# Kernel optimization log

Measured on AMD Instinct MI355X. Metric: run time of the kernel, lower is better.

Reference implementation:

```python
import jax, jax.numpy as jnp
import numpy as np

N = 20000   # nodes
IN = 128    # in_feats
H = 2       # n_heads
D = 32      # per-head dim (hid_feats = H*D = 64)
K = 3       # diffusion hops in AGDNConv
R = 5       # relations into dst type 'drug'
E = 320000  # edges per relation
NEG_SLOPE = 0.2


def setup_inputs() -> dict:
    key = jax.random.key(0)
    ks = jax.random.split(key, 11)
    s = 1.0 / np.sqrt(IN)
    return dict(
        h=jax.random.normal(ks[0], (N, IN), jnp.float32),
        src_idx=jax.random.randint(ks[1], (R, E), 0, N, dtype=jnp.int32),
        dst_idx=jax.random.randint(ks[2], (R, E), 0, N, dtype=jnp.int32),
        fc_w=jax.random.normal(ks[3], (R, IN, H * D), jnp.float32) * s,
        res_w=jax.random.normal(ks[4], (R, IN, H * D), jnp.float32) * s,
        attn_l=jax.random.normal(ks[5], (R, H, D), jnp.float32) * 0.1,
        attn_r=jax.random.normal(ks[6], (R, H, D), jnp.float32) * 0.1,
        hop_attn_l=jax.random.normal(ks[7], (R, H, D), jnp.float32) * 0.1,
        hop_attn_r=jax.random.normal(ks[8], (R, H, D), jnp.float32) * 0.1,
        w_rel=jax.random.normal(ks[9], (R, R), jnp.float32) * (1.0 / np.sqrt(R)),
        b_rel=jax.random.normal(ks[10], (R,), jnp.float32) * 0.1,
    )


def _agdn_conv(h, src, dst, fc_w, res_w, al, ar, hal, har):
    """One AGDNConv (GAT attention + K-hop diffusion + HA hop attention + residual)."""
    x = (h @ fc_w).reshape(N, H, D)                       # [N,H,D] projected feats
    el = jnp.sum(x * al, -1)                              # [N,H]
    er = jnp.sum(x * ar, -1)                              # [N,H]
    e = jax.nn.leaky_relu(el[src] + er[dst], NEG_SLOPE)   # [E,H] edge logits
    # segment softmax over incoming edges per dst node
    emax = jax.ops.segment_max(e, dst, num_segments=N)
    emax = jnp.where(jnp.isfinite(emax), emax, 0.0)
    ee = jnp.exp(e - emax[dst])
    denom = jax.ops.segment_sum(ee, dst, num_segments=N)
    alpha = ee / jnp.maximum(denom[dst], 1e-9)            # [E,H]

    def hop(hk, _):
        msg = alpha[:, :, None] * hk[src]                 # [E,H,D] gather+weight
        hk1 = jax.ops.segment_sum(msg, dst, num_segments=N)
        return hk1, hk1

    _, hks = jax.lax.scan(hop, x, None, length=K)         # [K,N,H,D]
    hops = jnp.concatenate([x[None], hks], axis=0)        # [K+1,N,H,D]
    # hop_norm: L2 normalize each hop's features
    hops = hops / jnp.maximum(jnp.linalg.norm(hops, axis=-1, keepdims=True), 1e-9)
    # HA hop attention
    hl = jnp.sum(hops * hal, -1)                          # [K+1,N,H]
    hr = jnp.sum(hops[0] * har, -1)                       # [N,H]
    hop_w = jax.nn.softmax(jax.nn.leaky_relu(hl + hr[None], NEG_SLOPE), axis=0)
    out = jnp.einsum('knh,knhd->nhd', hop_w, hops)        # [N,H,D]
    return out + (h @ res_w).reshape(N, H, D)             # residual


def reference(h, src_idx, dst_idx, fc_w, res_w, attn_l, attn_r, hop_attn_l, hop_attn_r, w_rel, b_rel):
    # per-relation AGDN convolutions (HeteroGraphConv dispatch)
    outs = jax.vmap(_agdn_conv, in_axes=(None, 0, 0, 0, 0, 0, 0, 0, 0))(
        h, src_idx, dst_idx, fc_w, res_w, attn_l, attn_r, hop_attn_l, hop_attn_r)  # [R,N,H,D]
    # my_agg_func2: learned relation weights = model_drug(ones(R))
    weights = w_rel @ jnp.ones((R,), jnp.float32) + b_rel  # [R]
    combined = jnp.einsum('r,rnhd->nhd', weights, outs)    # weighted relation sum
    return jnp.mean(combined, axis=1)                      # combine='mean' over heads -> [N,D]
```

## Files before the change

kernel.cpp:

```cpp
#include <hip/hip_runtime.h>
#include <hip/hip_bf16.h>

#define NN 20000
#define IN 128
#define HH 2
#define DD 32
#define HD 64
#define KK 3
#define RR 5
#define EE 320000
#define NEG 0.2f

#define PADK 136
#define NB 313
#define NBLK 64
#define CHUNK 5000
#define CAP 2048
#define NBCAP (NB * CAP)
#define RPS 20004
#define HTOT (NN * IN / 4)

typedef short v8s __attribute__((ext_vector_type(8)));
typedef float v4f __attribute__((ext_vector_type(4)));
typedef _Float16 hf8 __attribute__((ext_vector_type(8)));

__device__ __forceinline__ ushort f2b(float f) {
    unsigned u = __float_as_uint(f);
    unsigned r = (u + 0x7fff + ((u >> 16) & 1)) >> 16;
    return (ushort)r;
}
__device__ __forceinline__ ushort f2h(float f) {
    _Float16 h = (_Float16)f;
    return __builtin_bit_cast(ushort, h);
}
__device__ __forceinline__ float h2f(ushort u) {
    _Float16 h = __builtin_bit_cast(_Float16, u);
    return (float)h;
}
__device__ __forceinline__ float2 up2(unsigned u) {
    return make_float2(h2f((ushort)(u & 0xFFFF)), h2f((ushort)(u >> 16)));
}

__global__ __launch_bounds__(256) void cvt_kernel(
    const float* __restrict__ h, const float* __restrict__ fcw,
    const float* __restrict__ resw, ushort* __restrict__ wb,
    ushort* __restrict__ hb, int* __restrict__ bcnt)
{
    int j = blockIdx.x * 256 + threadIdx.x;
    if (j < RR * NB) bcnt[j] = 0;
    if (j < RR * 128 * IN) {
        int k = j & 127;
        int c = (j >> 7) & 127;
        int r = j >> 14;
        float v = (c < HD) ? fcw[(r * IN + k) * HD + c] : resw[(r * IN + k) * HD + (c - HD)];
        wb[j] = f2b(v);
    }
    int t = j - RR * 128 * IN;
    if (t >= 0 && t < HTOT) {
        float4 v = ((const float4*)h)[t];
        ((ushort4*)hb)[t] = make_ushort4(f2b(v.x), f2b(v.y), f2b(v.z), f2b(v.w));
    }
}

__global__ __launch_bounds__(256) void proj_mfma(
    const ushort* __restrict__ hb, const ushort* __restrict__ wb,
    const float* __restrict__ attn_l, const float* __restrict__ attn_r,
    ushort* __restrict__ t0, ushort* __restrict__ resh,
    float* __restrict__ el, float* __restrict__ er)
{
    __shared__ ushort As[64 * PADK];
    __shared__ ushort Bs[128 * PADK];
    int bx = blockIdx.x;
    int r = bx / 313;
    int tile = bx - r * 313;
    int n0 = tile * 64;
    int tid = threadIdx.x;

    #pragma unroll
    for (int i = 0; i < 4; i++) {
        int c = tid + 256 * i;
        int row = c >> 4;
        int off = (c & 15) * 8;
        int gn = n0 + row;
        uint4 v = make_uint4(0u, 0u, 0u, 0u);
        if (gn < NN) v = *(const uint4*)&hb[(size_t)gn * IN + off];
        *(uint4*)&As[row * PADK + off] = v;
    }
    const ushort* wr = wb + (size_t)r * 128 * IN;
    #pragma unroll
    for (int i = 0; i < 8; i++) {
        int c = tid + 256 * i;
        int row = c >> 4;
        int off = (c & 15) * 8;
        *(uint4*)&Bs[row * PADK + off] = *(const uint4*)&wr[row * IN + off];
    }
    __syncthreads();

    int w = tid >> 6, lane = tid & 63;
    int lm = lane & 15, lq = lane >> 4;

    v4f acc[4][2];
    #pragma unroll
    for (int mt = 0; mt < 4; mt++)
        #pragma unroll
        for (int nt = 0; nt < 2; nt++) acc[mt][nt] = (v4f){0.f, 0.f, 0.f, 0.f};

    const ushort* Ab = &As[lm * PADK + lq * 8];
    const ushort* Bb = &Bs[(w * 32 + lm) * PADK + lq * 8];

    #pragma unroll
    for (int ks = 0; ks < 4; ks++) {
        v8s a[4], b[2];
        #pragma unroll
        for (int mt = 0; mt < 4; mt++) a[mt] = *(const v8s*)(Ab + mt * 16 * PADK + ks * 32);
        #pragma unroll
        for (int nt = 0; nt < 2; nt++) b[nt] = *(const v8s*)(Bb + nt * 16 * PADK + ks * 32);
        #pragma unroll
        for (int mt = 0; mt < 4; mt++)
            #pragma unroll
            for (int nt = 0; nt < 2; nt++)
                acc[mt][nt] = __builtin_amdgcn_mfma_f32_16x16x32_bf16(a[mt], b[nt], acc[mt][nt], 0, 0, 0);
    }

    int colbase = w * 32 + lm;
    #pragma unroll
    for (int mt = 0; mt < 4; mt++) {
        #pragma unroll
        for (int nt = 0; nt < 2; nt++) {
            int col = colbase + nt * 16;
            #pragma unroll
            for (int p = 0; p < 4; p++) {
                int node = n0 + mt * 16 + lq * 4 + p;
                if (node < NN) {
                    float v = acc[mt][nt][p];
                    if (col < HD) {
                        t0[((size_t)r * NN + node) * HD + col] = f2h(v);
                    } else {
                        resh[((size_t)r * NN + node) * HD + (col - HD)] = f2h(v);
                    }
                }
            }
        }
    }

    if (w < 2) {
        float al0 = attn_l[(r * HH + w) * DD + lm];
        float al1 = attn_l[(r * HH + w) * DD + lm + 16];
        float ar0 = attn_r[(r * HH + w) * DD + lm];
        float ar1 = attn_r[(r * HH + w) * DD + lm + 16];
        #pragma unroll
        for (int mt = 0; mt < 4; mt++) {
            #pragma unroll
            for (int p = 0; p < 4; p++) {
                float pl = acc[mt][0][p] * al0 + acc[mt][1][p] * al1;
                float pr = acc[mt][0][p] * ar0 + acc[mt][1][p] * ar1;
                #pragma unroll
                for (int off = 1; off < 16; off <<= 1) {
                    pl += __shfl_xor(pl, off, 64);
                    pr += __shfl_xor(pr, off, 64);
                }
                if (lm == 0) {
                    int node = n0 + mt * 16 + lq * 4 + p;
                    if (node < NN) {
                        el[((size_t)r * NN + node) * HH + w] = pl;
                        er[((size_t)r * NN + node) * HH + w] = pr;
                    }
                }
            }
        }
    }
}

__global__ __launch_bounds__(256) void part_kernel(
    const int* __restrict__ src, const int* __restrict__ dst,
    int* __restrict__ bcnt, unsigned* __restrict__ bucketRec)
{
    __shared__ int hh[NB];
    int r = blockIdx.x >> 6;
    int blk = blockIdx.x & 63;
    int tid = threadIdx.x;
    for (int i = tid; i < NB; i += 256) hh[i] = 0;
    __syncthreads();
    const int* S = src + (size_t)r * EE + blk * CHUNK;
    const int* D = dst + (size_t)r * EE + blk * CHUNK;
    for (int i = tid; i < CHUNK; i += 256)
        atomicAdd(&hh[D[i] >> 6], 1);
    __syncthreads();
    for (int i = tid; i < NB; i += 256) {
        int c = hh[i];
        hh[i] = c ? atomicAdd(&bcnt[r * NB + i], c) : 0;
    }
    __syncthreads();
    unsigned* BR = bucketRec + (size_t)r * NBCAP;
    for (int i = tid; i < CHUNK; i += 256) {
        int s = S[i], d = D[i];
        int b = d >> 6;
        int pos = atomicAdd(&hh[b], 1);
        if (pos < CAP)
            BR[((size_t)b << 11) + pos] = (unsigned)s | ((unsigned)(d & 63) << 15);
    }
}

__global__ __launch_bounds__(256) void bsort_alpha_kernel(
    const unsigned* __restrict__ bucketRec, const int* __restrict__ bcnt,
    const float* __restrict__ el, const float* __restrict__ er,
    uint2* __restrict__ csrE, int* __restrict__ rowp)
{
    __shared__ int cnt64s[4][64];
    __shared__ int segS[65];
    __shared__ int cur[64];
    __shared__ float2 erL[64];
    __shared__ float2 mx2[64];
    __shared__ float2 inv2[64];
    __shared__ unsigned sSD[CAP];
    __shared__ unsigned sL[CAP];

    int bk = blockIdx.x;
    int r = bk / NB;
    int bkt = bk - r * NB;
    int tid = threadIdx.x;
    int wv = tid >> 6;
    int cnt = bcnt[bk];
    if (cnt > CAP) cnt = CAP;

    if (tid < 64) {
        cnt64s[0][tid] = 0; cnt64s[1][tid] = 0;
        cnt64s[2][tid] = 0; cnt64s[3][tid] = 0;
        int gn = bkt * 64 + tid;
        erL[tid] = (gn < NN) ? ((const float2*)er)[(size_t)r * NN + gn]
                             : make_float2(0.f, 0.f);
    }
    __syncthreads();
    const unsigned* BR = bucketRec + (size_t)bk * CAP;
    for (int i = tid; i < cnt; i += 256)
        atomicAdd(&cnt64s[wv][(BR[i] >> 15) & 63], 1);
    __syncthreads();
    if (tid < 64) {
        int v = cnt64s[0][tid] + cnt64s[1][tid] + cnt64s[2][tid] + cnt64s[3][tid];
        int x = v;
        #pragma unroll
        for (int off = 1; off < 64; off <<= 1) {
            int tt = __shfl_up(x, off, 64);
            if (tid >= off) x += tt;
        }
        segS[tid] = x - v;
        cur[tid] = x - v;
        if (tid == 63) segS[64] = x;
    }
    __syncthreads();
    const float2* el2 = (const float2*)el + (size_t)r * NN;
    for (int i = tid; i < cnt; i += 256) {
        unsigned rec = BR[i];
        int s = rec & 0x7FFF;
        int d = (rec >> 15) & 63;
        float2 a = el2[s];
        float2 b = erL[d];
        float l0 = a.x + b.x; l0 = l0 > 0.f ? l0 : NEG * l0;
        float l1 = a.y + b.y; l1 = l1 > 0.f ? l1 : NEG * l1;
        int pos = atomicAdd(&cur[d], 1);
        sSD[pos] = rec;
        sL[pos] = (unsigned)f2h(l0) | ((unsigned)f2h(l1) << 16);
    }
    __syncthreads();
    {
        int d = tid >> 2, sub = tid & 3;
        int b0 = segS[d], e0 = segS[d + 1];
        float m0 = -1e30f, m1 = -1e30f;
        for (int i = b0 + sub; i < e0; i += 4) {
            float2 l = up2(sL[i]);
            m0 = fmaxf(m0, l.x); m1 = fmaxf(m1, l.y);
        }
        m0 = fmaxf(m0, __shfl_xor(m0, 1, 64));
        m0 = fmaxf(m0, __shfl_xor(m0, 2, 64));
        m1 = fmaxf(m1, __shfl_xor(m1, 1, 64));
        m1 = fmaxf(m1, __shfl_xor(m1, 2, 64));
        float s0 = 0.f, s1 = 0.f;
        for (int i = b0 + sub; i < e0; i += 4) {
            float2 l = up2(sL[i]);
            s0 += __expf(l.x - m0); s1 += __expf(l.y - m1);
        }
        s0 += __shfl_xor(s0, 1, 64); s0 += __shfl_xor(s0, 2, 64);
        s1 += __shfl_xor(s1, 1, 64); s1 += __shfl_xor(s1, 2, 64);
        if (sub == 0) {
            mx2[d] = make_float2(m0, m1);
            inv2[d] = make_float2(1.f / fmaxf(s0, 1e-9f), 1.f / fmaxf(s1, 1e-9f));
            int gn = bkt * 64 + d;
            if (gn < NN) {
                int len = e0 - b0;
                rowp[r * RPS + gn] = (int)(((unsigned)(bkt * CAP + b0)) | ((unsigned)len << 20));
            }
        }
    }
    __syncthreads();
    uint2* E = csrE + (size_t)bk * CAP;
    for (int i = tid; i < cnt; i += 256) {
        unsigned rec = sSD[i];
        int d = (rec >> 15) & 63;
        float2 l = up2(sL[i]);
        float w0 = __expf(l.x - mx2[d].x) * inv2[d].x;
        float w1 = __expf(l.y - mx2[d].y) * inv2[d].y;
        E[i] = make_uint2(rec, (unsigned)f2h(w0) | ((unsigned)f2h(w1) << 16));
    }
}

__global__ __launch_bounds__(256) void hop_kernel(
    const ushort* __restrict__ tin, ushort* __restrict__ tout,
    const uint2* __restrict__ csrE, const int* __restrict__ rowp)
{
    int nbk = gridDim.x;
    int q = nbk >> 3, rmd = nbk & 7;
    int xcd = blockIdx.x & 7, pos = blockIdx.x >> 3;
    int bid = (xcd < rmd ? xcd * (q + 1) : rmd * (q + 1) + (xcd - rmd) * q) + pos;

    int w = (bid * 256 + (int)threadIdx.x) >> 6;
    if (w >= RR * (NN / 8)) return;
    int lane = threadIdx.x & 63;
    int g = lane >> 3;
    int f = (lane & 7) * 8;
    int sh = ((lane >> 2) & 1) * 16;
    int r = w / (NN / 8);
    int n0 = (w - r * (NN / 8)) * 8;

    unsigned pv = (unsigned)rowp[r * RPS + n0 + g];
    int bg = (int)(pv & 0xFFFFF);
    int len = (int)(pv >> 20);
    int eg = bg + len;
    int cl = (len + 1) >> 1;
    int b2 = bg + cl;

    int lastA = bg + cl - 1;
    lastA = lastA > bg ? lastA : bg;
    int lastB = eg - 1;
    lastB = lastB > b2 ? lastB : b2;

    const ushort* T = tin + (size_t)r * NN * HD;
    const uint2* E = csrE + (size_t)r * NBCAP;

    int iA1 = bg + 1 < lastA ? bg + 1 : lastA;
    int iB1 = b2 + 1 < lastB ? b2 + 1 : lastB;
    uint2 raC = E[lastA < bg ? lastA : bg], rbC = E[b2 < lastB ? b2 : lastB];
    uint2 raN = E[iA1], rbN = E[iB1];
    int na0 = (int)(raC.x & 0x7FFF); na0 = na0 < NN ? na0 : 0;
    int nb0 = (int)(rbC.x & 0x7FFF); nb0 = nb0 < NN ? nb0 : 0;
    hf8 fa = *(const hf8*)&T[(size_t)na0 * HD + f];
    hf8 fb = *(const hf8*)&T[(size_t)nb0 * HD + f];

    float accA[8] = {0.f, 0.f, 0.f, 0.f, 0.f, 0.f, 0.f, 0.f};
    float accB[8] = {0.f, 0.f, 0.f, 0.f, 0.f, 0.f, 0.f, 0.f};
    #pragma unroll 2
    for (int j = 0; j < cl; j++) {
        int ja = bg + j + 2; ja = ja < lastA ? ja : lastA;
        int jb = b2 + j + 2; jb = jb < lastB ? jb : lastB;
        uint2 ra2 = E[ja];
        uint2 rb2 = E[jb];
        int na1 = (int)(raN.x & 0x7FFF); na1 = na1 < NN ? na1 : 0;
        int nb1 = (int)(rbN.x & 0x7FFF); nb1 = nb1 < NN ? nb1 : 0;
        hf8 fa1 = *(const hf8*)&T[(size_t)na1 * HD + f];
        hf8 fb1 = *(const hf8*)&T[(size_t)nb1 * HD + f];
        float wa = h2f((ushort)(raC.y >> sh));
        float wb = (b2 + j < eg) ? h2f((ushort)(rbC.y >> sh)) : 0.f;
        #pragma unroll
        for (int k2 = 0; k2 < 8; k2++) {
            accA[k2] += wa * (float)fa[k2];
            accB[k2] += wb * (float)fb[k2];
        }
        raC = raN; raN = ra2;
        rbC = rbN; rbN = rb2;
        fa = fa1; fb = fb1;
    }
    ushort o[8];
    #pragma unroll
    for (int k = 0; k < 8; k++) o[k] = f2h(accA[k] + accB[k]);
    *(uint4*)&tout[((size_t)r * NN + n0 + g) * HD + f] = *(uint4*)o;
}

__global__ __launch_bounds__(256) void final_kernel(
    const ushort* __restrict__ t0, const ushort* __restrict__ t1,
    const ushort* __restrict__ t2, const ushort* __restrict__ t3,
    const ushort* __restrict__ resh,
    const float* __restrict__ hal, const float* __restrict__ har,
    const float* __restrict__ w_rel, const float* __restrict__ b_rel,
    float* __restrict__ out)
{
    int idx = blockIdx.x * 256 + threadIdx.x;
    if (idx >= NN * HH * 4) return;
    int fq = idx & 3;
    int h_ = (idx >> 2) & 1;
    int n = idx >> 3;
    const ushort* tb[4] = {t0, t1, t2, t3};
    float o[8];
    #pragma unroll
    for (int d = 0; d < 8; d++) o[d] = 0.f;

    for (int r = 0; r < RR; r++) {
        float wr = b_rel[r];
        #pragma unroll
        for (int j = 0; j < RR; j++) wr += w_rel[r * RR + j];
        const float* hp = hal + (r * HH + h_) * DD + fq * 8;
        const float* gp = har + (r * HH + h_) * DD + fq * 8;
        float4 ha0 = *(const float4*)hp;
        float4 ha1 = *(const float4*)(hp + 4);
        float4 hr0 = *(const float4*)gp;
        float4 hr1 = *(const float4*)(gp + 4);
        float halc[8] = {ha0.x, ha0.y, ha0.z, ha0.w, ha1.x, ha1.y, ha1.z, ha1.w};
        float harc[8] = {hr0.x, hr0.y, hr0.z, hr0.w, hr1.x, hr1.y, hr1.z, hr1.w};

        size_t tbase = ((size_t)r * NN + n) * HD + h_ * DD + fq * 8;
        uint4 tv[4];
        float sq[4], dl[4], dr = 0.f;
        #pragma unroll
        for (int k = 0; k < 4; k++) {
            tv[k] = *(const uint4*)(tb[k] + tbase);
            unsigned ww[4] = {tv[k].x, tv[k].y, tv[k].z, tv[k].w};
            float s = 0.f, d1 = 0.f;
            #pragma unroll
            for (int j = 0; j < 4; j++) {
                float2 v = up2(ww[j]);
                s  += v.x * v.x + v.y * v.y;
                d1 += v.x * halc[2 * j] + v.y * halc[2 * j + 1];
                if (k == 0)
                    dr += v.x * harc[2 * j] + v.y * harc[2 * j + 1];
            }
            sq[k] = s; dl[k] = d1;
        }
        #pragma unroll
        for (int k = 0; k < 4; k++) {
            sq[k] += __shfl_xor(sq[k], 1, 64); sq[k] += __shfl_xor(sq[k], 2, 64);
            dl[k] += __shfl_xor(dl[k], 1, 64); dl[k] += __shfl_xor(dl[k], 2, 64);
        }
        dr += __shfl_xor(dr, 1, 64); dr += __shfl_xor(dr, 2, 64);

        float inv[4], lg[4], mx = -1e30f;
        #pragma unroll
        for (int k = 0; k < 4; k++)
            inv[k] = 1.f / fmaxf(sqrtf(sq[k]), 1e-9f);
        #pragma unroll
        for (int k = 0; k < 4; k++) {
            float l = dl[k] * inv[k] + dr * inv[0];
            l = l > 0.f ? l : NEG * l;
            lg[k] = l;
            mx = fmaxf(mx, l);
        }
        float ssum = 0.f;
        #pragma unroll
        for (int k = 0; k < 4; k++) { lg[k] = __expf(lg[k] - mx); ssum += lg[k]; }
        float sw = wr / ssum;
        #pragma unroll
        for (int k = 0; k < 4; k++) {
            float coef = lg[k] * inv[k] * sw;
            unsigned ww[4] = {tv[k].x, tv[k].y, tv[k].z, tv[k].w};
            #pragma unroll
            for (int j = 0; j < 4; j++) {
                float2 v = up2(ww[j]);
                o[2 * j]     += coef * v.x;
                o[2 * j + 1] += coef * v.y;
            }
        }
        uint4 rv = *(const uint4*)(resh + tbase);
        unsigned rw[4] = {rv.x, rv.y, rv.z, rv.w};
        #pragma unroll
        for (int j = 0; j < 4; j++) {
            float2 v = up2(rw[j]);
            o[2 * j]     += wr * v.x;
            o[2 * j + 1] += wr * v.y;
        }
    }
    float p[8];
    #pragma unroll
    for (int j = 0; j < 8; j++) p[j] = __shfl_down(o[j], 4, 64);
    if (h_ == 0) {
        float4* op = (float4*)(out + (size_t)n * DD + fq * 8);
        op[0] = make_float4(0.5f * (o[0] + p[0]), 0.5f * (o[1] + p[1]),
                            0.5f * (o[2] + p[2]), 0.5f * (o[3] + p[3]));
        op[1] = make_float4(0.5f * (o[4] + p[4]), 0.5f * (o[5] + p[5]),
                            0.5f * (o[6] + p[6]), 0.5f * (o[7] + p[7]));
    }
}

extern "C" void kernel_launch(void* const* d_in, const int* in_sizes, int n_in,
                              void* d_out, int out_size, void* d_ws, size_t ws_size,
                              hipStream_t stream) {
    (void)in_sizes; (void)n_in; (void)out_size; (void)ws_size;
    const float* h     = (const float*)d_in[0];
    const int*   src   = (const int*)d_in[1];
    const int*   dst   = (const int*)d_in[2];
    const float* fcw   = (const float*)d_in[3];
    const float* resw  = (const float*)d_in[4];
    const float* atl   = (const float*)d_in[5];
    const float* atr   = (const float*)d_in[6];
    const float* hal   = (const float*)d_in[7];
    const float* har   = (const float*)d_in[8];
    const float* wrel  = (const float*)d_in[9];
    const float* brel  = (const float*)d_in[10];
    float* out = (float*)d_out;

    float* ws = (float*)d_ws;
    size_t off = 0;
    float* el   = ws + off;  off += (size_t)RR * NN * HH;
    float* er   = ws + off;  off += (size_t)RR * NN * HH;
    uint2* csrE = (uint2*)(ws + off);      off += (size_t)RR * NBCAP * 2;
    unsigned* bucketRec = (unsigned*)(ws + off); off += (size_t)RR * NBCAP;
    ushort* resh = (ushort*)(ws + off);    off += (size_t)RR * NN * HD / 2;
    ushort* t0  = (ushort*)(ws + off);     off += (size_t)RR * NN * HD / 2;
    ushort* t1  = (ushort*)(ws + off);     off += (size_t)RR * NN * HD / 2;
    ushort* t2  = (ushort*)(ws + off);     off += (size_t)RR * NN * HD / 2;
    ushort* t3  = (ushort*)(ws + off);     off += (size_t)RR * NN * HD / 2;
    ushort* wb  = (ushort*)(ws + off);     off += (size_t)RR * 128 * IN / 2;
    ushort* hb  = (ushort*)(ws + off);     off += (size_t)NN * IN / 2;
    int* rowp   = (int*)(ws + off);  off += (size_t)RR * RPS;
    int* bcnt   = (int*)(ws + off);  off += (size_t)RR * NB;

    cvt_kernel<<<(RR * 128 * IN + HTOT + 255) / 256, 256, 0, stream>>>(h, fcw, resw, wb, hb, bcnt);
    proj_mfma<<<313 * RR, 256, 0, stream>>>(hb, wb, atl, atr, t0, resh, el, er);
    part_kernel<<<RR * NBLK, 256, 0, stream>>>(src, dst, bcnt, bucketRec);
    bsort_alpha_kernel<<<RR * NB, 256, 0, stream>>>(bucketRec, bcnt, el, er, csrE, rowp);
    hop_kernel<<<(RR * (NN / 8) + 3) / 4, 256, 0, stream>>>(t0, t1, csrE, rowp);
    hop_kernel<<<(RR * (NN / 8) + 3) / 4, 256, 0, stream>>>(t1, t2, csrE, rowp);
    hop_kernel<<<(RR * (NN / 8) + 3) / 4, 256, 0, stream>>>(t2, t3, csrE, rowp);
    final_kernel<<<(NN * HH * 4 + 255) / 256, 256, 0, stream>>>(t0, t1, t2, t3, resh, hal, har, wrel, brel, out);
}
```

Measured before the change: 236.0 us.

## Fuse partitioning into projection and first hop into bucket sort, pad CSR pairs

```diff
diff --git a/kernel.cpp b/kernel.cpp
--- a/kernel.cpp
+++ b/kernel.cpp
@@ -19,6 +19,7 @@
 #define NBCAP (NB * CAP)
 #define RPS 20004
 #define HTOT (NN * IN / 4)
+#define PARTB (RR * NBLK)
 
 typedef short v8s __attribute__((ext_vector_type(8)));
 typedef float v4f __attribute__((ext_vector_type(4)));
@@ -62,19 +63,49 @@
     }
 }
 
-__global__ __launch_bounds__(256) void proj_mfma(
+__global__ __launch_bounds__(256) void projpart_kernel(
     const ushort* __restrict__ hb, const ushort* __restrict__ wb,
     const float* __restrict__ attn_l, const float* __restrict__ attn_r,
     ushort* __restrict__ t0, ushort* __restrict__ resh,
-    float* __restrict__ el, float* __restrict__ er)
+    float* __restrict__ el, float* __restrict__ er,
+    const int* __restrict__ src, const int* __restrict__ dst,
+    int* __restrict__ bcnt, unsigned* __restrict__ bucketRec)
 {
     __shared__ ushort As[64 * PADK];
     __shared__ ushort Bs[128 * PADK];
-    int bx = blockIdx.x;
+    int tid = threadIdx.x;
+
+    if (blockIdx.x < PARTB) {
+        int* hh = (int*)As;
+        int r = blockIdx.x >> 6;
+        int blk = blockIdx.x & 63;
+        for (int i = tid; i < NB; i += 256) hh[i] = 0;
+        __syncthreads();
+        const int* S = src + (size_t)r * EE + blk * CHUNK;
+        const int* D = dst + (size_t)r * EE + blk * CHUNK;
+        for (int i = tid; i < CHUNK; i += 256)
+            atomicAdd(&hh[D[i] >> 6], 1);
+        __syncthreads();
+        for (int i = tid; i < NB; i += 256) {
+            int c = hh[i];
+            hh[i] = c ? atomicAdd(&bcnt[r * NB + i], c) : 0;
+        }
+        __syncthreads();
+        unsigned* BR = bucketRec + (size_t)r * NBCAP;
+        for (int i = tid; i < CHUNK; i += 256) {
+            int s = S[i], d = D[i];
+            int b = d >> 6;
+            int pos = atomicAdd(&hh[b], 1);
+            if (pos < CAP)
+                BR[((size_t)b << 11) + pos] = (unsigned)s | ((unsigned)(d & 63) << 15);
+        }
+        return;
+    }
+
+    int bx = blockIdx.x - PARTB;
     int r = bx / 313;
     int tile = bx - r * 313;
     int n0 = tile * 64;
-    int tid = threadIdx.x;
 
     #pragma unroll
     for (int i = 0; i < 4; i++) {
@@ -171,44 +202,16 @@
     }
 }
 
-__global__ __launch_bounds__(256) void part_kernel(
-    const int* __restrict__ src, const int* __restrict__ dst,
-    int* __restrict__ bcnt, unsigned* __restrict__ bucketRec)
-{
-    __shared__ int hh[NB];
-    int r = blockIdx.x >> 6;
-    int blk = blockIdx.x & 63;
-    int tid = threadIdx.x;
-    for (int i = tid; i < NB; i += 256) hh[i] = 0;
-    __syncthreads();
-    const int* S = src + (size_t)r * EE + blk * CHUNK;
-    const int* D = dst + (size_t)r * EE + blk * CHUNK;
-    for (int i = tid; i < CHUNK; i += 256)
-        atomicAdd(&hh[D[i] >> 6], 1);
-    __syncthreads();
-    for (int i = tid; i < NB; i += 256) {
-        int c = hh[i];
-        hh[i] = c ? atomicAdd(&bcnt[r * NB + i], c) : 0;
-    }
-    __syncthreads();
-    unsigned* BR = bucketRec + (size_t)r * NBCAP;
-    for (int i = tid; i < CHUNK; i += 256) {
-        int s = S[i], d = D[i];
-        int b = d >> 6;
-        int pos = atomicAdd(&hh[b], 1);
-        if (pos < CAP)
-            BR[((size_t)b << 11) + pos] = (unsigned)s | ((unsigned)(d & 63) << 15);
-    }
-}
-
-__global__ __launch_bounds__(256) void bsort_alpha_kernel(
+__global__ __launch_bounds__(256) void bsort_alpha_hop1_kernel(
     const unsigned* __restrict__ bucketRec, const int* __restrict__ bcnt,
     const float* __restrict__ el, const float* __restrict__ er,
-    uint2* __restrict__ csrE, int* __restrict__ rowp)
+    const ushort* __restrict__ t0, uint2* __restrict__ csrE,
+    int* __restrict__ rowp, ushort* __restrict__ t1)
 {
     __shared__ int cnt64s[4][64];
     __shared__ int segS[65];
     __shared__ int cur[64];
+    __shared__ int pbS[64];
     __shared__ float2 erL[64];
     __shared__ float2 mx2[64];
     __shared__ float2 inv2[64];
@@ -221,7 +224,7 @@
     int tid = threadIdx.x;
     int wv = tid >> 6;
     int cnt = bcnt[bk];
-    if (cnt > CAP) cnt = CAP;
+    if (cnt > CAP - 64) cnt = CAP - 64;
 
     if (tid < 64) {
         cnt64s[0][tid] = 0; cnt64s[1][tid] = 0;
@@ -238,13 +241,16 @@
     if (tid < 64) {
         int v = cnt64s[0][tid] + cnt64s[1][tid] + cnt64s[2][tid] + cnt64s[3][tid];
         int x = v;
+        int y = v & 1;
         #pragma unroll
         for (int off = 1; off < 64; off <<= 1) {
-            int tt = __shfl_up(x, off, 64);
-            if (tid >= off) x += tt;
+            int tx = __shfl_up(x, off, 64);
+            int ty = __shfl_up(y, off, 64);
+            if (tid >= off) { x += tx; y += ty; }
         }
         segS[tid] = x - v;
-        cur[tid] = x - v;
+        cur[tid]  = x - v;
+        pbS[tid]  = (x - v) + (y - (v & 1));
         if (tid == 63) segS[64] = x;
     }
     __syncthreads();
@@ -287,7 +293,8 @@
             int gn = bkt * 64 + d;
             if (gn < NN) {
                 int len = e0 - b0;
-                rowp[r * RPS + gn] = (int)(((unsigned)(bkt * CAP + b0)) | ((unsigned)len << 20));
+                rowp[r * RPS + gn] =
+                    (int)(((unsigned)(bkt * CAP + pbS[d])) | ((unsigned)len << 20));
             }
         }
     }
@@ -299,7 +306,48 @@
         float2 l = up2(sL[i]);
         float w0 = __expf(l.x - mx2[d].x) * inv2[d].x;
         float w1 = __expf(l.y - mx2[d].y) * inv2[d].y;
-        E[i] = make_uint2(rec, (unsigned)f2h(w0) | ((unsigned)f2h(w1) << 16));
+        unsigned wp = (unsigned)f2h(w0) | ((unsigned)f2h(w1) << 16);
+        E[pbS[d] + (i - segS[d])] = make_uint2(rec, wp);
+        sL[i] = wp;
+    }
+    if (tid < 64) {
+        int len = segS[tid + 1] - segS[tid];
+        if (len & 1) E[pbS[tid] + len] = make_uint2(0u, 0u);
+    }
+    __syncthreads();
+
+    int lane = tid & 63;
+    int g = lane >> 3;
+    int f = (lane & 7) * 8;
+    int sh = ((lane >> 2) & 1) * 16;
+    const ushort* T0 = t0 + (size_t)r * NN * HD;
+    #pragma unroll
+    for (int half = 0; half < 2; half++) {
+        int d = half * 32 + wv * 8 + g;
+        int b0 = segS[d];
+        int len = segS[d + 1] - b0;
+        float acc[8] = {0.f, 0.f, 0.f, 0.f, 0.f, 0.f, 0.f, 0.f};
+        if (len > 0) {
+            float wC = h2f((ushort)(sL[b0] >> sh));
+            int sC = sSD[b0] & 0x7FFF;
+            hf8 fC = *(const hf8*)&T0[(size_t)sC * HD + f];
+            for (int j = 0; j < len; j++) {
+                int jn = j + 1 < len ? j + 1 : len - 1;
+                float wN = h2f((ushort)(sL[b0 + jn] >> sh));
+                int sN = sSD[b0 + jn] & 0x7FFF;
+                hf8 fN = *(const hf8*)&T0[(size_t)sN * HD + f];
+                #pragma unroll
+                for (int k = 0; k < 8; k++) acc[k] += wC * (float)fC[k];
+                wC = wN; fC = fN;
+            }
+        }
+        int node = bkt * 64 + d;
+        if (node < NN) {
+            ushort o[8];
+            #pragma unroll
+            for (int k = 0; k < 8; k++) o[k] = f2h(acc[k]);
+            *(uint4*)&t1[((size_t)r * NN + node) * HD + f] = *(uint4*)o;
+        }
     }
 }
 
@@ -324,53 +372,42 @@
     unsigned pv = (unsigned)rowp[r * RPS + n0 + g];
     int bg = (int)(pv & 0xFFFFF);
     int len = (int)(pv >> 20);
-    int eg = bg + len;
-    int cl = (len + 1) >> 1;
-    int b2 = bg + cl;
-
-    int lastA = bg + cl - 1;
-    lastA = lastA > bg ? lastA : bg;
-    int lastB = eg - 1;
-    lastB = lastB > b2 ? lastB : b2;
+    int pairs = (len + 1) >> 1;
+    int lastP = pairs > 0 ? pairs - 1 : 0;
 
     const ushort* T = tin + (size_t)r * NN * HD;
-    const uint2* E = csrE + (size_t)r * NBCAP;
-
-    int iA1 = bg + 1 < lastA ? bg + 1 : lastA;
-    int iB1 = b2 + 1 < lastB ? b2 + 1 : lastB;
-    uint2 raC = E[lastA < bg ? lastA : bg], rbC = E[b2 < lastB ? b2 : lastB];
-    uint2 raN = E[iA1], rbN = E[iB1];
-    int na0 = (int)(raC.x & 0x7FFF); na0 = na0 < NN ? na0 : 0;
-    int nb0 = (int)(rbC.x & 0x7FFF); nb0 = nb0 < NN ? nb0 : 0;
-    hf8 fa = *(const hf8*)&T[(size_t)na0 * HD + f];
-    hf8 fb = *(const hf8*)&T[(size_t)nb0 * HD + f];
-
-    float accA[8] = {0.f, 0.f, 0.f, 0.f, 0.f, 0.f, 0.f, 0.f};
-    float accB[8] = {0.f, 0.f, 0.f, 0.f, 0.f, 0.f, 0.f, 0.f};
+    const uint4* E4 = (const uint4*)(csrE + (size_t)r * NBCAP);
+    int base4 = bg >> 1;
+
+    uint4 rC = E4[base4];
+    uint4 rN = E4[base4 + (1 < pairs ? 1 : lastP)];
+    int s0 = (int)(rC.x & 0x7FFF); s0 = s0 < NN ? s0 : 0;
+    int s1 = (int)(rC.z & 0x7FFF); s1 = s1 < NN ? s1 : 0;
+    hf8 f0 = *(const hf8*)&T[(size_t)s0 * HD + f];
+    hf8 f1 = *(const hf8*)&T[(size_t)s1 * HD + f];
+
+    float acc[8] = {0.f, 0.f, 0.f, 0.f, 0.f, 0.f, 0.f, 0.f};
     #pragma unroll 2
-    for (int j = 0; j < cl; j++) {
-        int ja = bg + j + 2; ja = ja < lastA ? ja : lastA;
-        int jb = b2 + j + 2; jb = jb < lastB ? jb : lastB;
-        uint2 ra2 = E[ja];
-        uint2 rb2 = E[jb];
-        int na1 = (int)(raN.x & 0x7FFF); na1 = na1 < NN ? na1 : 0;
-        int nb1 = (int)(rbN.x & 0x7FFF); nb1 = nb1 < NN ? nb1 : 0;
-        hf8 fa1 = *(const hf8*)&T[(size_t)na1 * HD + f];
-        hf8 fb1 = *(const hf8*)&T[(size_t)nb1 * HD + f];
-        float wa = h2f((ushort)(raC.y >> sh));
-        float wb = (b2 + j < eg) ? h2f((ushort)(rbC.y >> sh)) : 0.f;
-        #pragma unroll
-        for (int k2 = 0; k2 < 8; k2++) {
-            accA[k2] += wa * (float)fa[k2];
-            accB[k2] += wb * (float)fb[k2];
-        }
-        raC = raN; raN = ra2;
-        rbC = rbN; rbN = rb2;
-        fa = fa1; fb = fb1;
+    for (int j = 0; j < pairs; j++) {
+        int j2 = j + 2 < pairs ? j + 2 : lastP;
+        uint4 r2 = E4[base4 + j2];
+        int n0i = (int)(rN.x & 0x7FFF); n0i = n0i < NN ? n0i : 0;
+        int n1i = (int)(rN.z & 0x7FFF); n1i = n1i < NN ? n1i : 0;
+        hf8 g0 = *(const hf8*)&T[(size_t)n0i * HD + f];
+        hf8 g1 = *(const hf8*)&T[(size_t)n1i * HD + f];
+        float w0 = h2f((ushort)(rC.y >> sh));
+        float w1 = h2f((ushort)(rC.w >> sh));
+        #pragma unroll
+        for (int k = 0; k < 8; k++) {
+            acc[k] += w0 * (float)f0[k];
+            acc[k] += w1 * (float)f1[k];
+        }
+        rC = rN; rN = r2;
+        f0 = g0; f1 = g1;
     }
     ushort o[8];
     #pragma unroll
-    for (int k = 0; k < 8; k++) o[k] = f2h(accA[k] + accB[k]);
+    for (int k = 0; k < 8; k++) o[k] = f2h(acc[k]);
     *(uint4*)&tout[((size_t)r * NN + n0 + g) * HD + f] = *(uint4*)o;
 }
 
@@ -511,10 +548,9 @@
     int* bcnt   = (int*)(ws + off);  off += (size_t)RR * NB;
 
     cvt_kernel<<<(RR * 128 * IN + HTOT + 255) / 256, 256, 0, stream>>>(h, fcw, resw, wb, hb, bcnt);
-    proj_mfma<<<313 * RR, 256, 0, stream>>>(hb, wb, atl, atr, t0, resh, el, er);
-    part_kernel<<<RR * NBLK, 256, 0, stream>>>(src, dst, bcnt, bucketRec);
-    bsort_alpha_kernel<<<RR * NB, 256, 0, stream>>>(bucketRec, bcnt, el, er, csrE, rowp);
-    hop_kernel<<<(RR * (NN / 8) + 3) / 4, 256, 0, stream>>>(t0, t1, csrE, rowp);
+    projpart_kernel<<<PARTB + 313 * RR, 256, 0, stream>>>(hb, wb, atl, atr, t0, resh, el, er,
+                                                          src, dst, bcnt, bucketRec);
+    bsort_alpha_hop1_kernel<<<RR * NB, 256, 0, stream>>>(bucketRec, bcnt, el, er, t0, csrE, rowp, t1);
     hop_kernel<<<(RR * (NN / 8) + 3) / 4, 256, 0, stream>>>(t1, t2, csrE, rowp);
     hop_kernel<<<(RR * (NN / 8) + 3) / 4, 256, 0, stream>>>(t2, t3, csrE, rowp);
     final_kernel<<<(NN * HH * 4 + 255) / 256, 256, 0, stream>>>(t0, t1, t2, t3, resh, hal, har, wrel, brel, out);
```

Measured after the change: 214.2 us. 1.1x faster.
